# Performance work log

Measured on AMD Instinct MI355X. Metric: run time of the kernel, lower is better.

Reference implementation:

```python
import jax, jax.numpy as jnp
import numpy as np


def setup_inputs() -> dict:
    key = jax.random.key(0)
    k1, k2 = jax.random.split(key)
    B, IN, OUT = 4096, 4096, 4096
    x = jax.random.normal(k1, (B, IN), dtype=jnp.float32)
    W = jax.random.normal(k2, (OUT, IN), dtype=jnp.float32) * (1.0 / np.sqrt(IN))
    return {"x": x, "W": W, "k": 128}


def reference(x, W, k):
    # temp = (x[:, None, :] * W).sum(axis=1)  ==  x * W.sum(axis=0)  -> [B, in]
    # (the original materializes the O(B*out*in) intermediate; math is identical)
    temp = jax.lax.stop_gradient(x) * jnp.sum(W, axis=0)  # x_vals is detached in torch
    _, idx_top = jax.lax.top_k(jnp.abs(temp), k)          # [B, k] indices into `in` dim
    B = x.shape[0]
    z = jnp.ones_like(x).at[jnp.arange(B)[:, None], idx_top].set(0.0)
    out = jnp.matmul(x * z, W.T)                          # [B, out]
    return out
```

## Files before the change

### kernel.cpp

```cpp
#include <hip/hip_runtime.h>
#include <hip/hip_bf16.h>
#include <stdint.h>

#define B_DIM   4096
#define IN_DIM  4096
#define OUT_DIM 4096
#define K_SEL   128

typedef unsigned short u16;
typedef __bf16 bf16x8 __attribute__((ext_vector_type(8)));
typedef float  f32x4  __attribute__((ext_vector_type(4)));

static __device__ __forceinline__ u16 f2bf(float f) {
    uint32_t u = __builtin_bit_cast(uint32_t, f);
    uint32_t r = (u + 0x7fffu + ((u >> 16) & 1u)) >> 16;
    return (u16)r;
}

__global__ __launch_bounds__(256) void colsum_conv(const float* __restrict__ W,
                                                   double* __restrict__ part,
                                                   u16* __restrict__ Wb) {
    int cb = blockIdx.x & 15;
    int rb = blockIdx.x >> 4;
    int col = cb * 256 + threadIdx.x;
    int row0 = rb * 256;
    double s = 0.0;
    for (int r = 0; r < 256; ++r) {
        size_t idx = (size_t)(row0 + r) * IN_DIM + col;
        float v = W[idx];
        s += (double)v;
        Wb[idx] = f2bf(v);
    }
    part[(size_t)rb * IN_DIM + col] = s;
}

__global__ __launch_bounds__(256) void colsum_final(const double* __restrict__ part,
                                                    float* __restrict__ cs) {
    int col = blockIdx.x * 256 + threadIdx.x;
    double s = 0.0;
    for (int r = 0; r < 16; ++r) s += part[(size_t)r * IN_DIM + col];
    cs[col] = (float)s;
}

__global__ __launch_bounds__(256) void topk_mask(const float* __restrict__ x,
                                                 const float* __restrict__ cs,
                                                 u16* __restrict__ xz) {
    __shared__ uint32_t hist[256];
    __shared__ uint32_t suf[256];
    __shared__ uint32_t s_scan[256];
    __shared__ uint32_t s_prefix, s_krem;

    const int b = blockIdx.x, t = threadIdx.x;
    const float4* xrow = (const float4*)(x + (size_t)b * IN_DIM);
    const float4* csv  = (const float4*)cs;

    float    xr[16];
    uint32_t ul[16];
#pragma unroll
    for (int q = 0; q < 4; ++q) {
        float4 xv = xrow[t * 4 + q];
        float4 cv = csv[t * 4 + q];
        xr[q*4+0] = xv.x; xr[q*4+1] = xv.y; xr[q*4+2] = xv.z; xr[q*4+3] = xv.w;
        ul[q*4+0] = __builtin_bit_cast(uint32_t, xv.x * cv.x) & 0x7fffffffu;
        ul[q*4+1] = __builtin_bit_cast(uint32_t, xv.y * cv.y) & 0x7fffffffu;
        ul[q*4+2] = __builtin_bit_cast(uint32_t, xv.z * cv.z) & 0x7fffffffu;
        ul[q*4+3] = __builtin_bit_cast(uint32_t, xv.w * cv.w) & 0x7fffffffu;
    }
    if (t == 0) { s_prefix = 0u; s_krem = K_SEL; }
    __syncthreads();

#pragma unroll
    for (int p = 3; p >= 0; --p) {
        const int sh = p * 8;
        const uint32_t hi_mask = (p == 3) ? 0u : (0xFFFFFFFFu << (sh + 8));
        const uint32_t prefix = s_prefix;
        const uint32_t krem   = s_krem;
        hist[t] = 0u;
        __syncthreads();
#pragma unroll
        for (int j = 0; j < 16; ++j) {
            uint32_t u = ul[j];
            if ((u & hi_mask) == (prefix & hi_mask))
                atomicAdd(&hist[(u >> sh) & 255u], 1u);
        }
        __syncthreads();
        uint32_t mine = hist[t];
        suf[t] = mine;
        __syncthreads();
#pragma unroll
        for (int off = 1; off < 256; off <<= 1) {
            uint32_t other = (t + off < 256) ? suf[t + off] : 0u;
            __syncthreads();
            mine += other;
            suf[t] = mine;
            __syncthreads();
        }
        uint32_t mysuf   = suf[t];
        uint32_t nextsuf = (t < 255) ? suf[t + 1] : 0u;
        if (mysuf >= krem && (t == 255 || nextsuf < krem)) {
            s_prefix = prefix | ((uint32_t)t << sh);
            s_krem   = krem - nextsuf;
        }
        __syncthreads();
    }
    const uint32_t T       = s_prefix;
    const uint32_t need_eq = s_krem;

    int cnt = 0;
#pragma unroll
    for (int j = 0; j < 16; ++j) cnt += (ul[j] == T) ? 1 : 0;
    s_scan[t] = (uint32_t)cnt;
    __syncthreads();
    uint32_t inc = (uint32_t)cnt;
#pragma unroll
    for (int off = 1; off < 256; off <<= 1) {
        uint32_t other = (t >= off) ? s_scan[t - off] : 0u;
        __syncthreads();
        inc += other;
        s_scan[t] = inc;
        __syncthreads();
    }
    const int base = (int)(inc - (uint32_t)cnt);

    union { u16 us[16]; uint4 v[2]; } ob;
    int eqseen = 0;
#pragma unroll
    for (int j = 0; j < 16; ++j) {
        uint32_t u = ul[j];
        bool drop = (u > T);
        if (u == T) {
            if (base + eqseen < (int)need_eq) drop = true;
            ++eqseen;
        }
        ob.us[j] = drop ? (u16)0 : f2bf(xr[j]);
    }
    uint4* dst = (uint4*)(xz + (size_t)b * IN_DIM + t * 16);
    dst[0] = ob.v[0];
    dst[1] = ob.v[1];
}

#define NT 64

__global__ __launch_bounds__(512, 2) void gemm_8ph(const u16* __restrict__ A,
                                                   const u16* __restrict__ Bm,
                                                   float* __restrict__ C) {
    __shared__ u16 lds_[2 * 4 * 8192];

    const int bid = blockIdx.x;
    const int swz = (bid & 7) * 32 + (bid >> 3);
    const int m0 = (swz >> 4) * 256, n0 = (swz & 15) * 256;

    const int t = threadIdx.x;
    const int w = t >> 6, l = t & 63;
    const int lr = l & 15, lk = l >> 4;
    const int wm = w >> 2, wn = w & 3;

    const int e3   = (lr & 7) << 3;
    const int col0 = (lk << 3) ^ e3;
    const int cswz = ((l & 7) ^ (l >> 3)) * 8;

    f32x4 acc[8][4];
#pragma unroll
    for (int i = 0; i < 8; ++i)
#pragma unroll
        for (int j = 0; j < 4; ++j) acc[i][j] = f32x4{0.f, 0.f, 0.f, 0.f};

#define GLOAD(g, off_bytes)                                                     \
    __builtin_amdgcn_global_load_lds(                                           \
        (const __attribute__((address_space(1))) void*)(g),                     \
        (__attribute__((address_space(3))) void*)(((char*)lds_) + (off_bytes)), \
        16, 0, 0)

    auto stageA = [&](int bufn, int j, int q, int kt) {
        int off = ((bufn * 4 + j) * 16384) + q * 8192 + w * 1024;
        const u16* g = A + (size_t)(m0 + j * 128 + q * 64 + w * 8 + (l >> 3)) * IN_DIM
                         + kt + cswz;
        GLOAD(g, off);
    };
    auto stageB = [&](int bufn, int qn, int j, int kt) {
        int off = ((bufn * 4 + 2 + qn) * 16384) + j * 8192 + w * 1024;
        const u16* g = Bm + (size_t)(n0 + (j * 2 + (w >> 2)) * 64 + qn * 32
                                     + (w & 3) * 8 + (l >> 3)) * IN_DIM
                          + kt + cswz;
        GLOAD(g, off);
    };

    stageA(0, 0, 0, 0);  stageA(0, 1, 0, 0);
    stageA(0, 0, 1, 0);  stageA(0, 1, 1, 0);
    stageB(0, 0, 0, 0);  stageB(0, 0, 1, 0);
    stageB(0, 1, 0, 0);  stageB(0, 1, 1, 0);
    stageA(1, 0, 0, 64); stageA(1, 1, 0, 64);
    stageB(1, 0, 0, 64); stageB(1, 0, 1, 64);
    asm volatile("s_waitcnt vmcnt(4)" ::: "memory");
    __builtin_amdgcn_s_barrier();
    asm volatile("" ::: "memory");

    for (int u = 0; u < NT; ++u) {
        const int buf = u & 1, bufn = buf ^ 1;
        const int kt1 = (u + 1) * 64, kt2 = (u + 2) * 64;
        const int regA = (buf * 4 + wm) * 8192 + lr * 64;
#pragma unroll
        for (int p = 0; p < 4; ++p) {
            const int qm = p >> 1, qn = p & 1;
            bf16x8 a[4][2], b[2][2];
            const int ra = regA + qm * 4096;
#pragma unroll
            for (int mi = 0; mi < 4; ++mi) {
                a[mi][0] = *(const bf16x8*)&lds_[ra + mi * 1024 + col0];
                a[mi][1] = *(const bf16x8*)&lds_[ra + mi * 1024 + (col0 ^ 32)];
            }
            const int rbq = (buf * 4 + 2 + qn) * 8192 + (wn * 32 + lr) * 64;
#pragma unroll
            for (int ni = 0; ni < 2; ++ni) {
                b[ni][0] = *(const bf16x8*)&lds_[rbq + ni * 1024 + col0];
                b[ni][1] = *(const bf16x8*)&lds_[rbq + ni * 1024 + (col0 ^ 32)];
            }
            if (p == 0)      { if (u < NT - 1) { stageA(bufn, 0, 1, kt1); stageA(bufn, 1, 1, kt1); } }
            else if (p == 1) { if (u < NT - 1) { stageB(bufn, 1, 0, kt1); stageB(bufn, 1, 1, kt1); } }
            else if (p == 2) { if (u < NT - 2) { stageA(buf,  0, 0, kt2); stageA(buf,  1, 0, kt2); } }
            else             { if (u < NT - 2) { stageB(buf,  0, 0, kt2); stageB(buf,  0, 1, kt2); } }
            asm volatile("" ::: "memory");
            __builtin_amdgcn_s_barrier();
            asm volatile("s_waitcnt lgkmcnt(0)" ::: "memory");
            __builtin_amdgcn_sched_barrier(0);
            __builtin_amdgcn_s_setprio(1);
#pragma unroll
            for (int mi = 0; mi < 4; ++mi)
#pragma unroll
                for (int ni = 0; ni < 2; ++ni) {
                    acc[qm*4+mi][qn*2+ni] = __builtin_amdgcn_mfma_f32_16x16x32_bf16(
                        a[mi][0], b[ni][0], acc[qm*4+mi][qn*2+ni], 0, 0, 0);
                    acc[qm*4+mi][qn*2+ni] = __builtin_amdgcn_mfma_f32_16x16x32_bf16(
                        a[mi][1], b[ni][1], acc[qm*4+mi][qn*2+ni], 0, 0, 0);
                }
            __builtin_amdgcn_s_setprio(0);
            __builtin_amdgcn_sched_barrier(0);
            if (p == 0 || p == 3) {
                asm volatile("s_waitcnt vmcnt(6)" ::: "memory");
            }
            asm volatile("" ::: "memory");
            __builtin_amdgcn_s_barrier();
            asm volatile("" ::: "memory");
        }
    }
#undef GLOAD

#pragma unroll
    for (int gmi = 0; gmi < 8; ++gmi)
#pragma unroll
        for (int gni = 0; gni < 4; ++gni)
#pragma unroll
            for (int r = 0; r < 4; ++r) {
                int row = m0 + wm * 128 + gmi * 16 + lk * 4 + r;
                int col = n0 + wn * 64 + gni * 16 + lr;
                C[(size_t)row * OUT_DIM + col] = acc[gmi][gni][r];
            }
}

extern "C" void kernel_launch(void* const* d_in, const int* in_sizes, int n_in,
                              void* d_out, int out_size, void* d_ws, size_t ws_size,
                              hipStream_t stream) {
    const float* x = (const float*)d_in[0];
    const float* W = (const float*)d_in[1];
    float* out = (float*)d_out;

    char* ws = (char*)d_ws;
    u16*    Wb   = (u16*)ws;
    u16*    xz   = (u16*)(ws + (size_t)32 * 1024 * 1024);
    float*  cs   = (float*)(ws + (size_t)64 * 1024 * 1024);
    double* part = (double*)(ws + (size_t)64 * 1024 * 1024 + 16 * 1024);

    colsum_conv<<<256, 256, 0, stream>>>(W, part, Wb);
    colsum_final<<<16, 256, 0, stream>>>(part, cs);
    topk_mask<<<4096, 256, 0, stream>>>(x, cs, xz);
    gemm_8ph<<<256, 512, 0, stream>>>(xz, Wb, out);
}
```

Before: 211.6 us.

## Rework GEMM LDS staging schedule and widen colsum parallelism

Splits the W column-sum and bf16 conversion over 2048 blocks of 32 rows instead of 256 blocks of 256 rows, so the conversion pass has more memory parallelism. The partial sums now live in the output buffer, which is only overwritten later by the GEMM. The GEMM stages A and B tiles with a simpler per-thread contiguous layout and issues loads in a new order. Each phase now covers one k-half across all four N sub-tiles, and it waits for memory only once per iteration. The trade-off is a bigger final reduction (128 partials per column) and a different latency-hiding pattern. The clamped tail prefetch also issues redundant loads in the last iterations.

```diff
diff --git a/kernel.cpp b/kernel.cpp
--- a/kernel.cpp
+++ b/kernel.cpp
@@ -23,9 +23,9 @@
     int cb = blockIdx.x & 15;
     int rb = blockIdx.x >> 4;
     int col = cb * 256 + threadIdx.x;
-    int row0 = rb * 256;
+    int row0 = rb * 32;
     double s = 0.0;
-    for (int r = 0; r < 256; ++r) {
+    for (int r = 0; r < 32; ++r) {
         size_t idx = (size_t)(row0 + r) * IN_DIM + col;
         float v = W[idx];
         s += (double)v;
@@ -38,7 +38,7 @@
                                                     float* __restrict__ cs) {
     int col = blockIdx.x * 256 + threadIdx.x;
     double s = 0.0;
-    for (int r = 0; r < 16; ++r) s += part[(size_t)r * IN_DIM + col];
+    for (int r = 0; r < 128; ++r) s += part[(size_t)r * IN_DIM + col];
     cs[col] = (float)s;
 }
 
@@ -144,7 +144,7 @@
 __global__ __launch_bounds__(512, 2) void gemm_8ph(const u16* __restrict__ A,
                                                    const u16* __restrict__ Bm,
                                                    float* __restrict__ C) {
-    __shared__ u16 lds_[2 * 4 * 8192];
+    __shared__ u16 lds_[65536];
 
     const int bid = blockIdx.x;
     const int swz = (bid & 7) * 32 + (bid >> 3);
@@ -155,9 +155,8 @@
     const int lr = l & 15, lk = l >> 4;
     const int wm = w >> 2, wn = w & 3;
 
-    const int e3   = (lr & 7) << 3;
-    const int col0 = (lk << 3) ^ e3;
-    const int cswz = ((l & 7) ^ (l >> 3)) * 8;
+    const int cswz = ((t & 7) ^ ((t >> 3) & 7)) * 8;
+    const int colA = (lk * 8) ^ ((lr & 7) * 8);
 
     f32x4 acc[8][4];
 #pragma unroll
@@ -171,54 +170,50 @@
         (__attribute__((address_space(3))) void*)(((char*)lds_) + (off_bytes)), \
         16, 0, 0)
 
-    auto stageA = [&](int bufn, int j, int q, int kt) {
-        int off = ((bufn * 4 + j) * 16384) + q * 8192 + w * 1024;
-        const u16* g = A + (size_t)(m0 + j * 128 + q * 64 + w * 8 + (l >> 3)) * IN_DIM
-                         + kt + cswz;
-        GLOAD(g, off);
+    auto stA = [&](int kb, int s, int kt) {
+        GLOAD(A + (size_t)(m0 + s * 64 + (t >> 3)) * IN_DIM + kt + cswz,
+              kb * 65536 + s * 8192 + t * 16);
     };
-    auto stageB = [&](int bufn, int qn, int j, int kt) {
-        int off = ((bufn * 4 + 2 + qn) * 16384) + j * 8192 + w * 1024;
-        const u16* g = Bm + (size_t)(n0 + (j * 2 + (w >> 2)) * 64 + qn * 32
-                                     + (w & 3) * 8 + (l >> 3)) * IN_DIM
-                          + kt + cswz;
-        GLOAD(g, off);
+    auto stB = [&](int kb, int s, int kt) {
+        GLOAD(Bm + (size_t)(n0 + s * 64 + (t >> 3)) * IN_DIM + kt + cswz,
+              kb * 65536 + 32768 + s * 8192 + t * 16);
     };
 
-    stageA(0, 0, 0, 0);  stageA(0, 1, 0, 0);
-    stageA(0, 0, 1, 0);  stageA(0, 1, 1, 0);
-    stageB(0, 0, 0, 0);  stageB(0, 0, 1, 0);
-    stageB(0, 1, 0, 0);  stageB(0, 1, 1, 0);
-    stageA(1, 0, 0, 64); stageA(1, 1, 0, 64);
-    stageB(1, 0, 0, 64); stageB(1, 0, 1, 64);
-    asm volatile("s_waitcnt vmcnt(4)" ::: "memory");
+    stA(0, 0, 0); stA(0, 1, 0); stA(0, 2, 0); stA(0, 3, 0);
+    stB(0, 0, 0); stB(0, 1, 0); stB(0, 2, 0); stB(0, 3, 0);
+    stA(1, 0, 64); stA(1, 2, 64);
+    asm volatile("s_waitcnt vmcnt(2)" ::: "memory");
     __builtin_amdgcn_s_barrier();
     asm volatile("" ::: "memory");
 
-    for (int u = 0; u < NT; ++u) {
-        const int buf = u & 1, bufn = buf ^ 1;
-        const int kt1 = (u + 1) * 64, kt2 = (u + 2) * 64;
-        const int regA = (buf * 4 + wm) * 8192 + lr * 64;
+    for (int k = 0; k < NT; ++k) {
+        const int buf = k & 1, bufn = buf ^ 1;
+        const int kt1 = (k + 1) * 64;
+        const int ktc = (k + 2 < NT ? k + 2 : NT - 1) * 64;
+        const int Ab = buf * 32768 + (wm * 2) * 4096;
+        const int Bb = buf * 32768 + 16384 + wn * 4096;
 #pragma unroll
         for (int p = 0; p < 4; ++p) {
-            const int qm = p >> 1, qn = p & 1;
-            bf16x8 a[4][2], b[2][2];
-            const int ra = regA + qm * 4096;
-#pragma unroll
-            for (int mi = 0; mi < 4; ++mi) {
-                a[mi][0] = *(const bf16x8*)&lds_[ra + mi * 1024 + col0];
-                a[mi][1] = *(const bf16x8*)&lds_[ra + mi * 1024 + (col0 ^ 32)];
+            const int q = p >> 1, ks = p & 1;
+            const int col = colA ^ (ks * 32);
+            bf16x8 a[4], b[4];
+            const int ra = Ab + q * 4096 + lr * 64 + col;
+#pragma unroll
+            for (int mi = 0; mi < 4; ++mi)
+                a[mi] = *(const bf16x8*)&lds_[ra + mi * 1024];
+            const int rb = Bb + lr * 64 + col;
+#pragma unroll
+            for (int ni = 0; ni < 4; ++ni)
+                b[ni] = *(const bf16x8*)&lds_[rb + ni * 1024];
+
+            if (p == 0) {
+                if (k < NT - 1) { stB(bufn, 0, kt1); stB(bufn, 1, kt1);
+                                  stA(bufn, 1, kt1); stA(bufn, 3, kt1); }
+            } else if (p == 1) {
+                if (k < NT - 1) { stB(bufn, 2, kt1); stB(bufn, 3, kt1); }
+            } else if (p == 2) {
+                stA(buf, 0, ktc); stA(buf, 2, ktc);
             }
-            const int rbq = (buf * 4 + 2 + qn) * 8192 + (wn * 32 + lr) * 64;
-#pragma unroll
-            for (int ni = 0; ni < 2; ++ni) {
-                b[ni][0] = *(const bf16x8*)&lds_[rbq + ni * 1024 + col0];
-                b[ni][1] = *(const bf16x8*)&lds_[rbq + ni * 1024 + (col0 ^ 32)];
-            }
-            if (p == 0)      { if (u < NT - 1) { stageA(bufn, 0, 1, kt1); stageA(bufn, 1, 1, kt1); } }
-            else if (p == 1) { if (u < NT - 1) { stageB(bufn, 1, 0, kt1); stageB(bufn, 1, 1, kt1); } }
-            else if (p == 2) { if (u < NT - 2) { stageA(buf,  0, 0, kt2); stageA(buf,  1, 0, kt2); } }
-            else             { if (u < NT - 2) { stageB(buf,  0, 0, kt2); stageB(buf,  0, 1, kt2); } }
             asm volatile("" ::: "memory");
             __builtin_amdgcn_s_barrier();
             asm volatile("s_waitcnt lgkmcnt(0)" ::: "memory");
@@ -227,17 +222,12 @@
 #pragma unroll
             for (int mi = 0; mi < 4; ++mi)
 #pragma unroll
-                for (int ni = 0; ni < 2; ++ni) {
-                    acc[qm*4+mi][qn*2+ni] = __builtin_amdgcn_mfma_f32_16x16x32_bf16(
-                        a[mi][0], b[ni][0], acc[qm*4+mi][qn*2+ni], 0, 0, 0);
-                    acc[qm*4+mi][qn*2+ni] = __builtin_amdgcn_mfma_f32_16x16x32_bf16(
-                        a[mi][1], b[ni][1], acc[qm*4+mi][qn*2+ni], 0, 0, 0);
-                }
+                for (int ni = 0; ni < 4; ++ni)
+                    acc[q * 4 + mi][ni] = __builtin_amdgcn_mfma_f32_16x16x32_bf16(
+                        a[mi], b[ni], acc[q * 4 + mi][ni], 0, 0, 0);
             __builtin_amdgcn_s_setprio(0);
             __builtin_amdgcn_sched_barrier(0);
-            if (p == 0 || p == 3) {
-                asm volatile("s_waitcnt vmcnt(6)" ::: "memory");
-            }
+            if (p == 3) asm volatile("s_waitcnt vmcnt(2)" ::: "memory");
             asm volatile("" ::: "memory");
             __builtin_amdgcn_s_barrier();
             asm volatile("" ::: "memory");
@@ -248,12 +238,12 @@
 #pragma unroll
     for (int gmi = 0; gmi < 8; ++gmi)
 #pragma unroll
-        for (int gni = 0; gni < 4; ++gni)
+        for (int ni = 0; ni < 4; ++ni)
 #pragma unroll
             for (int r = 0; r < 4; ++r) {
-                int row = m0 + wm * 128 + gmi * 16 + lk * 4 + r;
-                int col = n0 + wn * 64 + gni * 16 + lr;
-                C[(size_t)row * OUT_DIM + col] = acc[gmi][gni][r];
+                int row = m0 + wm * 128 + (gmi >> 2) * 64 + (gmi & 3) * 16 + lk * 4 + r;
+                int col = n0 + wn * 64 + ni * 16 + lr;
+                C[(size_t)row * OUT_DIM + col] = acc[gmi][ni][r];
             }
 }
 
@@ -268,9 +258,9 @@
     u16*    Wb   = (u16*)ws;
     u16*    xz   = (u16*)(ws + (size_t)32 * 1024 * 1024);
     float*  cs   = (float*)(ws + (size_t)64 * 1024 * 1024);
-    double* part = (double*)(ws + (size_t)64 * 1024 * 1024 + 16 * 1024);
-
-    colsum_conv<<<256, 256, 0, stream>>>(W, part, Wb);
+    double* part = (double*)d_out;
+
+    colsum_conv<<<2048, 256, 0, stream>>>(W, part, Wb);
     colsum_final<<<16, 256, 0, stream>>>(part, cs);
     topk_mask<<<4096, 256, 0, stream>>>(x, cs, xz);
     gemm_8ph<<<256, 512, 0, stream>>>(xz, Wb, out);
```

Result: faster. 195.2 us (-7.8%).
